# Performance work log

Measured on AMD Instinct MI355X. Metric: run time of the kernel, lower is better.

The kernel has to match this reference:

```python
import jax, jax.numpy as jnp
import numpy as np

EMB_DIM = 4096
N_HEADS = 32
QKV_DIM = EMB_DIM // N_HEADS  # 128
B, S = 4, 4096


def setup_inputs() -> dict:
    key = jax.random.key(0)
    ks = jax.random.split(key, 7)
    std = 1.0 / np.sqrt(EMB_DIM)  # lecun-normal-ish init for DenseGeneral kernels
    x = jax.random.normal(ks[0], (B, S, EMB_DIM), dtype=jnp.float32)
    Wq = jax.random.normal(ks[1], (EMB_DIM, QKV_DIM, N_HEADS), dtype=jnp.float32) * std
    bq = jnp.zeros((QKV_DIM, N_HEADS), dtype=jnp.float32)
    Wk = jax.random.normal(ks[2], (EMB_DIM, QKV_DIM, 1), dtype=jnp.float32) * std
    bk = jnp.zeros((QKV_DIM, 1), dtype=jnp.float32)
    Wv = jax.random.normal(ks[3], (EMB_DIM, QKV_DIM, 1), dtype=jnp.float32) * std
    bv = jnp.zeros((QKV_DIM, 1), dtype=jnp.float32)
    return {"x": x, "Wq": Wq, "bq": bq, "Wk": Wk, "bk": bk, "Wv": Wv, "bv": bv}


def reference(x, Wq, bq, Wk, bk, Wv, bv):
    # q: (B, S, d, h) ; k, v: (B, S, d) -- single shared head (squeeze the 1-axis)
    q = jnp.einsum('bsD,Ddh->bsdh', x, Wq) + bq
    k = (jnp.einsum('bsD,Ddh->bsdh', x, Wk) + bk)[..., 0]
    v = (jnp.einsum('bsD,Ddh->bsdh', x, Wv) + bv)[..., 0]
    qkv_dim = q.shape[-2]
    n_heads = q.shape[-1]
    scale = 1.0 / jnp.sqrt(jnp.asarray(qkv_dim, dtype=q.dtype))
    # Original: scores = q @ swapaxes(repeat(k), -1, -2) -> contracts the HEADS
    # axis per token. With k repeated across heads this equals
    # (sum_h q[..., d, h]) * k[..., e]. einsum sums h (absent from output).
    scores = jnp.einsum('bsdh,bse->bsde', q, k) * scale  # (B, S, d, d)
    p = jax.nn.softmax(scores, axis=-1)
    # out[..., d, h] = sum_e p[..., d, e] * v_rep[..., e, h]; v identical per h.
    o = jnp.einsum('bsde,bse->bsd', p, v)  # (B, S, d)
    out = jnp.broadcast_to(o[..., None], o.shape + (n_heads,))  # (B, S, d, h)
    return out.reshape(x.shape[:-1] + (qkv_dim * n_heads,))
```

## Files before the change

### kernel.cpp

```cpp
#include <hip/hip_runtime.h>

#define EMB  4096
#define DH   128
#define NH   32
#define NTOK 16384
#define NCOL 384

#define BM 64
#define BK 64

typedef __attribute__((ext_vector_type(8))) short short8;
typedef __attribute__((ext_vector_type(4))) short short4_t;
typedef __attribute__((ext_vector_type(4))) float f32x4;

static __device__ __forceinline__ unsigned int cvt2(float a, float b) {
    unsigned int r;
    asm volatile("v_cvt_pk_bf16_f32 %0, %1, %2" : "=v"(r) : "v"(a), "v"(b));
    return r;
}
static __device__ __forceinline__ unsigned short f2bf(float f) {
    unsigned int u = __builtin_bit_cast(unsigned int, f);
    u += 0x7fffu + ((u >> 16) & 1u);
    return (unsigned short)(u >> 16);
}
static __device__ __forceinline__ float exp2_hw(float x) {
#if __has_builtin(__builtin_amdgcn_exp2f)
    return __builtin_amdgcn_exp2f(x);
#else
    float r;
    asm volatile("v_exp_f32 %0, %1\n\ts_nop 1" : "=v"(r) : "v"(x));
    return r;
#endif
}

__global__ void prep_w(const float* __restrict__ Wq, const float* __restrict__ bq,
                       const float* __restrict__ Wk, const float* __restrict__ bk,
                       const float* __restrict__ Wv, const float* __restrict__ bv,
                       unsigned short* __restrict__ W3F, float* __restrict__ bias) {
    const int tid = blockIdx.x * 256 + threadIdx.x;
    const int n  = tid >> 9;
    const int ck = tid & 511;
    const int D0 = ck * 8;

    float v[8];
    if (n < DH) {
#pragma unroll
        for (int e = 0; e < 8; ++e) {
            const float4* p = (const float4*)(Wq + (size_t)(D0 + e) * (DH * NH) + n * NH);
            float s = 0.f;
#pragma unroll
            for (int i = 0; i < 8; ++i) { float4 q = p[i]; s += (q.x + q.y) + (q.z + q.w); }
            v[e] = s;
        }
    } else if (n < 2 * DH) {
#pragma unroll
        for (int e = 0; e < 8; ++e) v[e] = Wk[(size_t)(D0 + e) * DH + (n - DH)];
    } else {
#pragma unroll
        for (int e = 0; e < 8; ++e) v[e] = Wv[(size_t)(D0 + e) * DH + (n - 2 * DH)];
    }

    union { short8 s; unsigned int u[4]; } pk;
#pragma unroll
    for (int j = 0; j < 4; ++j)
        pk.u[j] = (unsigned int)f2bf(v[2 * j]) | ((unsigned int)f2bf(v[2 * j + 1]) << 16);

    const int p    = n >> 6, r = n & 63;
    const int jfr  = r >> 4, lmod = r & 15;
    const int kt   = ck >> 3;
    const int kh   = (ck >> 2) & 1;
    const int lgrp = ck & 3;
    const int lane = lgrp * 16 + lmod;
    char* dst = (char*)W3F + (size_t)p * 524288 + (size_t)kt * 8192
              + (kh * 4 + jfr) * 1024 + lane * 16;
    *(short8*)dst = pk.s;

    if (ck == 0) {
        float b;
        if (n < DH) {
            float s = 0.f;
#pragma unroll
            for (int h = 0; h < NH; ++h) s += bq[n * NH + h];
            b = s;
        } else if (n < 2 * DH) {
            b = bk[n - DH];
        } else {
            b = bv[n - 2 * DH];
        }
        bias[n] = b;
    }
}

__global__ __launch_bounds__(384) void fused_mqa(const float* __restrict__ X,
                         const unsigned short* __restrict__ W3F,
                         const float* __restrict__ bias,
                         float* __restrict__ out) {
    __shared__ __align__(16) unsigned short Asm[BM * BK];
    __shared__ float qsm[32 * NCOL];

    const int bid  = blockIdx.x;
    const int wkid = (bid & 7) * 32 + (bid >> 3);
    const int m0   = wkid * BM;
    const int nt   = EMB / BK;

    const int t = threadIdx.x, lane = t & 63, w = t >> 6;
    const int lmod = lane & 15, lgrp = lane >> 4;

    f32x4 acc[4][4] = {};

    const int arow4 = lane >> 4;
    const float* xp = X + (size_t)(m0 + w * 16 + arow4) * EMB + (lane & 15) * 4;
    const int acs = (lane & 15) >> 1;
    const int ah4 = (lane & 1) * 4;

    const char* bsrc = (const char*)W3F + (size_t)w * 524288 + lane * 16;

    f32x4 av[4];

#define LOAD_AV(T) do { \
    _Pragma("unroll") \
    for (int i = 0; i < 4; ++i) \
        av[i] = __builtin_nontemporal_load((const f32x4*)(xp + (T) * BK + i * 4 * EMB)); \
} while (0)

#define WRITE_A() do { \
    _Pragma("unroll") \
    for (int idx = 0; idx < 4; ++idx) { \
        const int rl = w * 16 + idx * 4 + arow4; \
        union { short4_t s; unsigned int u[2]; } pk; \
        pk.u[0] = cvt2(av[idx].x, av[idx].y); \
        pk.u[1] = cvt2(av[idx].z, av[idx].w); \
        *(short4_t*)(&Asm[rl * BK + ((acs ^ (rl & 7)) << 3) + ah4]) = pk.s; \
    } \
} while (0)

    if (w < 4) LOAD_AV(0);

    for (int tt = 0; tt < nt; ++tt) {
        __syncthreads();
        if (w < 4) WRITE_A();
        __syncthreads();
        if (w < 4 && tt + 1 < nt) LOAD_AV(tt + 1);

        const char* bt = bsrc + (size_t)tt * 8192;
#pragma unroll
        for (int kh = 0; kh < 2; ++kh) {
            short8 af[4], bf[4];
#pragma unroll
            for (int j = 0; j < 4; ++j)
                bf[j] = *(const short8*)(bt + (kh * 4 + j) * 1024);
            const int cs = ((kh * 4 + lgrp) ^ (lmod & 7)) * 8;
#pragma unroll
            for (int i = 0; i < 4; ++i)
                af[i] = *(const short8*)(&Asm[(i * 16 + lmod) * BK + cs]);
#pragma unroll
            for (int i = 0; i < 4; ++i)
#pragma unroll
                for (int j = 0; j < 4; ++j)
                    acc[i][j] = __builtin_amdgcn_mfma_f32_16x16x32_bf16(af[i], bf[j], acc[i][j], 0, 0, 0);
        }
    }

    const float c = 0.088388347648318447f * 1.4426950408889634f;
#pragma unroll
    for (int pass = 0; pass < 2; ++pass) {
        __syncthreads();
#pragma unroll
        for (int j = 0; j < 4; ++j) {
            const int col = w * 64 + j * 16 + lmod;
            const float bj = bias[col];
#pragma unroll
            for (int i2 = 0; i2 < 2; ++i2) {
                const int row = i2 * 16 + (lgrp << 2);
#pragma unroll
                for (int r = 0; r < 4; ++r)
                    qsm[(row + r) * NCOL + col] = acc[pass * 2 + i2][j][r] + bj;
            }
        }
        __syncthreads();

        for (int tok = w; tok < 32; tok += 6) {
            const float* row = &qsm[tok * NCOL];
            const float q0  = row[lane],       q1  = row[64 + lane];
            const float kk0 = row[128 + lane], kk1 = row[192 + lane];

            float lmax = fmaxf(kk0, kk1), lmin = fminf(kk0, kk1);
#pragma unroll
            for (int off = 32; off; off >>= 1) {
                lmax = fmaxf(lmax, __shfl_xor(lmax, off));
                lmin = fminf(lmin, __shfl_xor(lmin, off));
            }

            const float a0 = q0 * c, a1 = q1 * c;
            const float m0v = (a0 >= 0.f) ? a0 * lmax : a0 * lmin;
            const float m1v = (a1 >= 0.f) ? a1 * lmax : a1 * lmin;

            float s00 = 0.f, s01 = 0.f, s10 = 0.f, s11 = 0.f;
#pragma unroll 8
            for (int e = 0; e < DH; ++e) {
                const float kv = row[128 + e];
                const float vv = row[256 + e];
                const float p0 = exp2_hw(fmaf(a0, kv, -m0v));
                const float p1 = exp2_hw(fmaf(a1, kv, -m1v));
                s00 += p0;  s01 = fmaf(p0, vv, s01);
                s10 += p1;  s11 = fmaf(p1, vv, s11);
            }
            const float o0 = s01 / s00;
            const float o1 = s11 / s10;

            float* orow = out + (size_t)(m0 + pass * 32 + tok) * (DH * NH);
#pragma unroll
            for (int it = 0; it < 16; ++it) {
                const int idx = it * 64 + lane;
                const int src = (it & 7) * 8 + (lane >> 3);
                const float val = (it < 8) ? __shfl(o0, src) : __shfl(o1, src);
                f32x4 f4 = {val, val, val, val};
                __builtin_nontemporal_store(f4, (f32x4*)(orow + idx * 4));
            }
        }
    }
#undef LOAD_AV
#undef WRITE_A
}

extern "C" void kernel_launch(void* const* d_in, const int* in_sizes, int n_in,
                              void* d_out, int out_size, void* d_ws, size_t ws_size,
                              hipStream_t stream) {
    const float* x  = (const float*)d_in[0];
    const float* Wq = (const float*)d_in[1];
    const float* bq = (const float*)d_in[2];
    const float* Wk = (const float*)d_in[3];
    const float* bk = (const float*)d_in[4];
    const float* Wv = (const float*)d_in[5];
    const float* bv = (const float*)d_in[6];
    float* out = (float*)d_out;

    char* ws = (char*)d_ws;
    unsigned short* W3F = (unsigned short*)ws;
    float* bias = (float*)(ws + 3145728);

    prep_w<<<(NCOL * 512) / 256, 256, 0, stream>>>(Wq, bq, Wk, bk, Wv, bv, W3F, bias);
    fused_mqa<<<NTOK / BM, 384, 0, stream>>>(x, W3F, bias, out);
}
```

Baseline: 182.6 us.

## Double-buffer X and weight fragment loads across K tiles with raw barriers

The K loop is unrolled by two, with ping-pong register buffers for the X tile (two tiles ahead) and for the weight B fragments (one tile ahead). Global loads are issued before the MFMA work on the current tile, so their latency can hide behind compute. __syncthreads is replaced with raw s_barrier plus an explicit lgkmcnt wait, which removes unneeded vmcnt waits on in-flight global loads. The cost is much higher register pressure from 16 short8 plus 8 f32x4 buffers, which could cause spills or lower occupancy. Out-of-range tiles are clamped, which adds some redundant loads at the tail.

Result: faster. 163.6 us (-10.4%).

```diff
diff --git a/kernel.cpp b/kernel.cpp
--- a/kernel.cpp
+++ b/kernel.cpp
@@ -115,50 +115,71 @@
 
     const char* bsrc = (const char*)W3F + (size_t)w * 524288 + lane * 16;
 
-    f32x4 av[4];
-
-#define LOAD_AV(T) do { \
+    f32x4 avA[4], avB[4];
+    short8 bfA[8], bfB[8];
+
+#define LOAD_AV(T, AV) do { \
+    const int tc_ = (T) < nt ? (T) : nt - 1; \
     _Pragma("unroll") \
     for (int i = 0; i < 4; ++i) \
-        av[i] = __builtin_nontemporal_load((const f32x4*)(xp + (T) * BK + i * 4 * EMB)); \
-} while (0)
-
-#define WRITE_A() do { \
+        AV[i] = __builtin_nontemporal_load((const f32x4*)(xp + tc_ * BK + i * 4 * EMB)); \
+} while (0)
+
+#define LOAD_BF(T, BF) do { \
+    const int tc_ = (T) < nt ? (T) : nt - 1; \
+    const char* bt_ = bsrc + (size_t)tc_ * 8192; \
+    _Pragma("unroll") \
+    for (int j = 0; j < 8; ++j) \
+        BF[j] = *(const short8*)(bt_ + j * 1024); \
+} while (0)
+
+#define WRITE_A(AV) do { \
     _Pragma("unroll") \
     for (int idx = 0; idx < 4; ++idx) { \
         const int rl = w * 16 + idx * 4 + arow4; \
         union { short4_t s; unsigned int u[2]; } pk; \
-        pk.u[0] = cvt2(av[idx].x, av[idx].y); \
-        pk.u[1] = cvt2(av[idx].z, av[idx].w); \
+        pk.u[0] = cvt2(AV[idx].x, AV[idx].y); \
+        pk.u[1] = cvt2(AV[idx].z, AV[idx].w); \
         *(short4_t*)(&Asm[rl * BK + ((acs ^ (rl & 7)) << 3) + ah4]) = pk.s; \
     } \
 } while (0)
 
-    if (w < 4) LOAD_AV(0);
-
-    for (int tt = 0; tt < nt; ++tt) {
-        __syncthreads();
-        if (w < 4) WRITE_A();
-        __syncthreads();
-        if (w < 4 && tt + 1 < nt) LOAD_AV(tt + 1);
-
-        const char* bt = bsrc + (size_t)tt * 8192;
-#pragma unroll
-        for (int kh = 0; kh < 2; ++kh) {
-            short8 af[4], bf[4];
-#pragma unroll
-            for (int j = 0; j < 4; ++j)
-                bf[j] = *(const short8*)(bt + (kh * 4 + j) * 1024);
-            const int cs = ((kh * 4 + lgrp) ^ (lmod & 7)) * 8;
-#pragma unroll
-            for (int i = 0; i < 4; ++i)
-                af[i] = *(const short8*)(&Asm[(i * 16 + lmod) * BK + cs]);
-#pragma unroll
-            for (int i = 0; i < 4; ++i)
-#pragma unroll
-                for (int j = 0; j < 4; ++j)
-                    acc[i][j] = __builtin_amdgcn_mfma_f32_16x16x32_bf16(af[i], bf[j], acc[i][j], 0, 0, 0);
-        }
+#define COMPUTE(BF) do { \
+    _Pragma("unroll") \
+    for (int kh = 0; kh < 2; ++kh) { \
+        const int cs = ((kh * 4 + lgrp) ^ (lmod & 7)) * 8; \
+        short8 af[4]; \
+        _Pragma("unroll") \
+        for (int i = 0; i < 4; ++i) \
+            af[i] = *(const short8*)(&Asm[(i * 16 + lmod) * BK + cs]); \
+        _Pragma("unroll") \
+        for (int i = 0; i < 4; ++i) \
+            _Pragma("unroll") \
+            for (int j = 0; j < 4; ++j) \
+                acc[i][j] = __builtin_amdgcn_mfma_f32_16x16x32_bf16(af[i], BF[kh * 4 + j], acc[i][j], 0, 0, 0); \
+    } \
+} while (0)
+
+#define ABAR()  do { __builtin_amdgcn_s_barrier(); } while (0)
+#define WBAR()  do { asm volatile("s_waitcnt lgkmcnt(0)" ::: "memory"); \
+                     __builtin_amdgcn_s_barrier(); } while (0)
+
+    if (w < 4) { LOAD_AV(0, avA); LOAD_AV(1, avB); }
+    LOAD_BF(0, bfA);
+
+    for (int tt = 0; tt < nt; tt += 2) {
+        ABAR();
+        if (w < 4) WRITE_A(avA);
+        WBAR();
+        LOAD_BF(tt + 1, bfB);
+        if (w < 4) LOAD_AV(tt + 2, avA);
+        COMPUTE(bfA);
+        ABAR();
+        if (w < 4) WRITE_A(avB);
+        WBAR();
+        LOAD_BF(tt + 2, bfA);
+        if (w < 4) LOAD_AV(tt + 3, avB);
+        COMPUTE(bfB);
     }
 
     const float c = 0.088388347648318447f * 1.4426950408889634f;
@@ -220,7 +241,11 @@
         }
     }
 #undef LOAD_AV
+#undef LOAD_BF
 #undef WRITE_A
+#undef COMPUTE
+#undef ABAR
+#undef WBAR
 }
 
 extern "C" void kernel_launch(void* const* d_in, const int* in_sizes, int n_in,
```
